# Kernel optimization log

Measured on AMD Instinct MI355X. Metric: run time of the kernel, lower is better.

## Reference

```python
import jax, jax.numpy as jnp
import numpy as np

B, S, DIM, HEADS = 4, 2048, 1024, 16
SCALE = float((DIM // HEADS) ** 0.5)  # sqrt(d_k) = 8.0
EPS = 1e-5


def _ln(h, g, b):
    m = jnp.mean(h, axis=-1, keepdims=True)
    v = jnp.mean((h - m) ** 2, axis=-1, keepdims=True)
    return (h - m) * jax.lax.rsqrt(v + EPS) * g + b


def setup_inputs() -> dict:
    key = jax.random.key(0)
    ks = jax.random.split(key, 16)
    w = lambda k: jax.random.normal(k, (DIM, DIM), jnp.float32) * 0.02
    vec = lambda k: jax.random.normal(k, (DIM,), jnp.float32) * 0.02
    return {
        "x": jax.random.normal(ks[0], (B, S, DIM), jnp.float32),
        "Wq": w(ks[1]), "bq": vec(ks[2]),
        "Wk": w(ks[3]), "bk": vec(ks[4]),
        "Wv": w(ks[5]), "bv": vec(ks[6]),
        "g_at": 1.0 + vec(ks[7]), "b_at": vec(ks[8]),
        "g_ln": 1.0 + vec(ks[9]), "b_ln": vec(ks[10]),
        "W1": w(ks[11]), "c1": vec(ks[12]),
        "W2": w(ks[13]), "c2": vec(ks[14]),
    }


def reference(x, Wq, bq, Wk, bk, Wv, bv, g_at, b_at, g_ln, b_ln, W1, c1, W2, c2):
    # --- MultiHeadAttention (single-head math: no head reshape in source) ---
    Q = x @ Wq + bq                                   # [B,S,D]
    K = x @ Wk + bk
    V = x @ Wv + bv
    scores = jax.nn.softmax(jnp.einsum('bqd,bkd->bqk', Q, K) / SCALE, axis=-1)
    at = _ln(jnp.einsum('bqk,bkd->bqd', scores, V) + x, g_at, b_at)
    # --- EncoderStack ---
    h = _ln(at + x, g_ln, b_ln)
    res = h
    # note: source's `if i != len(self.ffn)` is always True -> GELU on every layer
    h = jax.nn.gelu(h @ W1 + c1, approximate=False)
    h = jax.nn.gelu(h @ W2 + c2, approximate=False)
    return _ln(h + res, g_ln, b_ln)
```

## Files before the change

### kernel.cpp

```cpp
#include <hip/hip_runtime.h>
#include <cstdint>
#include <cstddef>

#define DIMN 1024
#define SEQ  2048
#define NBAT 4
#define TOKS (NBAT * SEQ)

typedef unsigned short u16;
typedef unsigned int   u32;

typedef __bf16 bf16x8 __attribute__((ext_vector_type(8)));
typedef float  f32x4  __attribute__((ext_vector_type(4)));

#define AS1 __attribute__((address_space(1)))
#define AS3 __attribute__((address_space(3)))


__device__ __forceinline__ u16 f2b(float f) {
  union { float f; u32 u; } v; v.f = f;
  u32 r = v.u + 0x7fffu + ((v.u >> 16) & 1u);
  return (u16)(r >> 16);
}

__device__ __forceinline__ float gelu_exact(float v) {
  return 0.5f * v * (1.0f + erff(v * 0.70710678118654752f));
}

__device__ __forceinline__ void blk_sum2(float& a, float& b, float* sm) {
  #pragma unroll
  for (int o = 32; o >= 1; o >>= 1) {
    a += __shfl_xor(a, o, 64);
    b += __shfl_xor(b, o, 64);
  }
  int w = threadIdx.x >> 6;
  if ((threadIdx.x & 63) == 0) { sm[w] = a; sm[4 + w] = b; }
  __syncthreads();
  a = sm[0] + sm[1] + sm[2] + sm[3];
  b = sm[4] + sm[5] + sm[6] + sm[7];
  __syncthreads();
}

__device__ __forceinline__ float blk_max(float a, float* sm) {
  #pragma unroll
  for (int o = 32; o >= 1; o >>= 1) a = fmaxf(a, __shfl_xor(a, o, 64));
  int w = threadIdx.x >> 6;
  if ((threadIdx.x & 63) == 0) sm[w] = a;
  __syncthreads();
  float r = fmaxf(fmaxf(sm[0], sm[1]), fmaxf(sm[2], sm[3]));
  __syncthreads();
  return r;
}

__device__ __forceinline__ float blk_sum1(float a, float* sm) {
  #pragma unroll
  for (int o = 32; o >= 1; o >>= 1) a += __shfl_xor(a, o, 64);
  int w = threadIdx.x >> 6;
  if ((threadIdx.x & 63) == 0) sm[w] = a;
  __syncthreads();
  float r = sm[0] + sm[1] + sm[2] + sm[3];
  __syncthreads();
  return r;
}


__global__ __launch_bounds__(256) void conv_x(const float* __restrict__ x,
                                              u16* __restrict__ xb) {
  size_t i = ((size_t)blockIdx.x * 256 + threadIdx.x) * 4;
  float4 v = *(const float4*)(x + i);
  uint2 o;
  o.x = (u32)f2b(v.x) | ((u32)f2b(v.y) << 16);
  o.y = (u32)f2b(v.z) | ((u32)f2b(v.w) << 16);
  *(uint2*)(xb + i) = o;
}

__global__ __launch_bounds__(256) void transpose_w5(
    const float* __restrict__ Wq, const float* __restrict__ Wk,
    const float* __restrict__ Wv, const float* __restrict__ W1,
    const float* __restrict__ W2,
    u16* __restrict__ WqT, u16* __restrict__ WkT, u16* __restrict__ WvT,
    u16* __restrict__ W1T, u16* __restrict__ W2T)
{
  const float* W; u16* T;
  switch (blockIdx.z) {
    case 0: W = Wq; T = WqT; break;
    case 1: W = Wk; T = WkT; break;
    case 2: W = Wv; T = WvT; break;
    case 3: W = W1; T = W1T; break;
    default: W = W2; T = W2T; break;
  }
  __shared__ float t[32][33];
  int tx = threadIdx.x, ty = threadIdx.y;
  int k0 = blockIdx.x * 32, n0 = blockIdx.y * 32;
  #pragma unroll
  for (int j = 0; j < 32; j += 8)
    t[ty + j][tx] = W[(size_t)(k0 + ty + j) * DIMN + n0 + tx];
  __syncthreads();
  #pragma unroll
  for (int j = 0; j < 32; j += 8)
    T[(size_t)(n0 + ty + j) * DIMN + k0 + tx] = f2b(t[tx][ty + j]);
}

template <int EPI>
__global__ __launch_bounds__(256) void gemm_bt(
    const u16* __restrict__ A, const u16* __restrict__ Bm,
    float* __restrict__ Cf, u16* __restrict__ Cb,
    const float* __restrict__ bias,
    int M, int N, int K, int ldc,
    size_t sA, size_t sB, size_t sC)
{
  __shared__ u16 As[128 * 64];
  __shared__ u16 Bs[128 * 64];

  const int tid  = threadIdx.x;
  const int bm0  = blockIdx.x * 128;
  const int bn0  = blockIdx.y * 128;
  A  += (size_t)blockIdx.z * sA;
  Bm += (size_t)blockIdx.z * sB;
  const int wave = tid >> 6, lane = tid & 63;
  const int wm   = (wave >> 1) * 64, wn = (wave & 1) * 64;
  const int l16  = lane & 15, quad = lane >> 4;

  f32x4 acc[4][4] = {};

  for (int k0 = 0; k0 < K; k0 += 64) {
    #pragma unroll
    for (int j = 0; j < 4; ++j) {
      const int c  = wave * 256 + j * 64 + lane;
      const int r  = c >> 3;
      const int cg = (c & 7) ^ (r & 7);
      const u16* gA = A  + (size_t)(bm0 + r) * K + k0 + cg * 8;
      const u16* gB = Bm + (size_t)(bn0 + r) * K + k0 + cg * 8;
      u16* lA = As + (wave * 4 + j) * 512;
      u16* lB = Bs + (wave * 4 + j) * 512;
      __builtin_amdgcn_global_load_lds((const AS1 void*)gA, (AS3 void*)lA, 16, 0, 0);
      __builtin_amdgcn_global_load_lds((const AS1 void*)gB, (AS3 void*)lB, 16, 0, 0);
    }
    __syncthreads();

    #pragma unroll
    for (int kk = 0; kk < 64; kk += 32) {
      const int kc = kk >> 3;
      const int sw = l16 & 7;
      bf16x8 af[4], bfr[4];
      #pragma unroll
      for (int t = 0; t < 4; ++t) {
        const int row = wm + t * 16 + l16;
        af[t] = *(const bf16x8*)(&As[row * 64 + (((kc + quad) ^ sw) << 3)]);
      }
      #pragma unroll
      for (int t = 0; t < 4; ++t) {
        const int row = wn + t * 16 + l16;
        bfr[t] = *(const bf16x8*)(&Bs[row * 64 + (((kc + quad) ^ sw) << 3)]);
      }
      #pragma unroll
      for (int mt = 0; mt < 4; ++mt)
        #pragma unroll
        for (int nt = 0; nt < 4; ++nt)
          acc[mt][nt] = __builtin_amdgcn_mfma_f32_16x16x32_bf16(
              af[mt], bfr[nt], acc[mt][nt], 0, 0, 0);
    }
    __syncthreads();
  }

  float* Cfz = Cf + (size_t)blockIdx.z * sC;
  u16*   Cbz = Cb + (size_t)blockIdx.z * sC;

  #pragma unroll
  for (int mt = 0; mt < 4; ++mt) {
    int grow0 = bm0 + wm + mt * 16 + quad * 4;
    #pragma unroll
    for (int nt = 0; nt < 4; ++nt) {
      int gcol = bn0 + wn + nt * 16 + l16;
      float bv = (EPI != 0) ? bias[gcol] : 0.0f;
      #pragma unroll
      for (int r = 0; r < 4; ++r) {
        float v  = acc[mt][nt][r] + bv;
        int grow = grow0 + r;
        if (EPI == 0) {
          Cfz[(size_t)grow * ldc + gcol] = v;
        } else if (EPI == 1) {
          Cbz[(size_t)grow * ldc + gcol] = f2b(v);
        } else if (EPI == 2) {
          Cbz[(size_t)((grow >> 11) * DIMN + gcol) * SEQ + (grow & 2047)] = f2b(v);
        } else if (EPI == 4) {
          Cbz[(size_t)grow * ldc + gcol] = f2b(gelu_exact(v));
        } else {
          Cfz[(size_t)grow * ldc + gcol] = gelu_exact(v);
        }
      }
    }
  }
}

__global__ __launch_bounds__(256) void softmax_rows(const float* __restrict__ Sc,
                                                    u16* __restrict__ P) {
  __shared__ float sm[8];
  int row = blockIdx.x, t = threadIdx.x;
  const float* s = Sc + (size_t)row * SEQ;
  float v[8];
  float mx = -1e30f;
  #pragma unroll
  for (int i = 0; i < 8; ++i) {
    v[i] = s[t + i * 256] * 0.125f;
    mx = fmaxf(mx, v[i]);
  }
  mx = blk_max(mx, sm);
  float sum = 0.0f;
  #pragma unroll
  for (int i = 0; i < 8; ++i) { v[i] = __expf(v[i] - mx); sum += v[i]; }
  sum = blk_sum1(sum, sm);
  float inv = 1.0f / sum;
  u16* p = P + (size_t)row * SEQ;
  #pragma unroll
  for (int i = 0; i < 8; ++i) p[t + i * 256] = f2b(v[i] * inv);
}

__global__ __launch_bounds__(256) void ln1_fused(
    const float* __restrict__ attn, const float* __restrict__ x,
    const float* __restrict__ g_at, const float* __restrict__ b_at,
    const float* __restrict__ g_ln, const float* __restrict__ b_ln,
    float* __restrict__ hres, u16* __restrict__ hb)
{
  __shared__ float sm[8];
  int row = blockIdx.x, t = threadIdx.x;
  size_t base = (size_t)row * DIMN;
  float y[4], xr[4];
  float s = 0.0f, s2 = 0.0f;
  #pragma unroll
  for (int i = 0; i < 4; ++i) {
    int c = t + i * 256;
    xr[i] = x[base + c];
    y[i]  = attn[base + c] + xr[i];
    s += y[i]; s2 += y[i] * y[i];
  }
  blk_sum2(s, s2, sm);
  float m  = s * (1.0f / DIMN);
  float rs = rsqrtf(s2 * (1.0f / DIMN) - m * m + 1e-5f);
  float z[4];
  s = 0.0f; s2 = 0.0f;
  #pragma unroll
  for (int i = 0; i < 4; ++i) {
    int c = t + i * 256;
    float at = (y[i] - m) * rs * g_at[c] + b_at[c];
    z[i] = at + xr[i];
    s += z[i]; s2 += z[i] * z[i];
  }
  blk_sum2(s, s2, sm);
  float m2  = s * (1.0f / DIMN);
  float rs2 = rsqrtf(s2 * (1.0f / DIMN) - m2 * m2 + 1e-5f);
  #pragma unroll
  for (int i = 0; i < 4; ++i) {
    int c = t + i * 256;
    float h = (z[i] - m2) * rs2 * g_ln[c] + b_ln[c];
    hres[base + c] = h;
    hb[base + c]   = f2b(h);
  }
}

__global__ __launch_bounds__(256) void ln2_final(
    const float* __restrict__ u, const float* __restrict__ hres,
    const float* __restrict__ g, const float* __restrict__ bb,
    float* __restrict__ out)
{
  __shared__ float sm[8];
  int row = blockIdx.x, t = threadIdx.x;
  size_t base = (size_t)row * DIMN;
  float y[4];
  float s = 0.0f, s2 = 0.0f;
  #pragma unroll
  for (int i = 0; i < 4; ++i) {
    int c = t + i * 256;
    y[i] = u[base + c] + hres[base + c];
    s += y[i]; s2 += y[i] * y[i];
  }
  blk_sum2(s, s2, sm);
  float m  = s * (1.0f / DIMN);
  float rs = rsqrtf(s2 * (1.0f / DIMN) - m * m + 1e-5f);
  #pragma unroll
  for (int i = 0; i < 4; ++i) {
    int c = t + i * 256;
    out[base + c] = (y[i] - m) * rs * g[c] + bb[c];
  }
}


extern "C" void kernel_launch(void* const* d_in, const int* in_sizes, int n_in,
                              void* d_out, int out_size, void* d_ws, size_t ws_size,
                              hipStream_t stream)
{
  const float* x    = (const float*)d_in[0];
  const float* Wq   = (const float*)d_in[1];
  const float* bq   = (const float*)d_in[2];
  const float* Wk   = (const float*)d_in[3];
  const float* bk   = (const float*)d_in[4];
  const float* Wv   = (const float*)d_in[5];
  const float* bv   = (const float*)d_in[6];
  const float* g_at = (const float*)d_in[7];
  const float* b_at = (const float*)d_in[8];
  const float* g_ln = (const float*)d_in[9];
  const float* b_ln = (const float*)d_in[10];
  const float* W1   = (const float*)d_in[11];
  const float* c1   = (const float*)d_in[12];
  const float* W2   = (const float*)d_in[13];
  const float* c2   = (const float*)d_in[14];
  float* out = (float*)d_out;

  char* ws = (char*)d_ws;
  const size_t MB = 1u << 20;
  const bool big = ws_size >= 172 * MB;

  u16* xb  = (u16*)(ws + 0 * MB);
  u16* W1T = (u16*)(ws + 16 * MB);
  u16* W2T = (u16*)(ws + 18 * MB);
  u16* WqT = (u16*)(ws + 20 * MB);
  u16* WkT = (u16*)(ws + 22 * MB);
  u16* WvT = (u16*)(ws + 24 * MB);
  u16* Qb  = (u16*)(ws + 26 * MB);
  u16* Kb  = (u16*)(ws + 42 * MB);
  u16* VT  = (u16*)(ws + 58 * MB);
  u16* hb  = Qb;
  u16* tb  = Kb;

  conv_x<<<(TOKS * DIMN) / 1024, 256, 0, stream>>>(x, xb);
  transpose_w5<<<dim3(32, 32, 5), dim3(32, 8), 0, stream>>>(
      Wq, Wk, Wv, W1, W2, WqT, WkT, WvT, W1T, W2T);

  gemm_bt<1><<<dim3(64, 8), 256, 0, stream>>>(xb, WqT, nullptr, Qb, bq,
                                              TOKS, DIMN, DIMN, DIMN, 0, 0, 0);
  gemm_bt<1><<<dim3(64, 8), 256, 0, stream>>>(xb, WkT, nullptr, Kb, bk,
                                              TOKS, DIMN, DIMN, DIMN, 0, 0, 0);
  gemm_bt<2><<<dim3(64, 8), 256, 0, stream>>>(xb, WvT, nullptr, VT, bv,
                                              TOKS, DIMN, DIMN, DIMN, 0, 0, 0);

  float* attn;
  float* hres;

  if (big) {
    float* Sc = (float*)(ws + 74 * MB);
    u16*   Pb = (u16*) (ws + 138 * MB);
    attn = (float*)(ws + 74 * MB);
    hres = (float*)(ws + 106 * MB);

    gemm_bt<0><<<dim3(16, 16, NBAT), 256, 0, stream>>>(
        Qb, Kb, Sc, nullptr, nullptr, SEQ, SEQ, DIMN, SEQ,
        (size_t)SEQ * DIMN, (size_t)SEQ * DIMN, (size_t)SEQ * SEQ);
    softmax_rows<<<TOKS, 256, 0, stream>>>(Sc, Pb);
    gemm_bt<0><<<dim3(16, 8, NBAT), 256, 0, stream>>>(
        Pb, VT, attn, nullptr, nullptr, SEQ, DIMN, SEQ, DIMN,
        (size_t)SEQ * SEQ, (size_t)DIMN * SEQ, (size_t)SEQ * DIMN);
  } else {
    float* Sc = (float*)(ws + 0 * MB);
    u16*   Pb = (u16*) (ws + 74 * MB);
    attn = (float*)(ws + 82 * MB);
    hres = (float*)(ws + 114 * MB);
    for (int b = 0; b < NBAT; ++b) {
      const size_t tok_off = (size_t)b * SEQ * DIMN;
      gemm_bt<0><<<dim3(16, 16), 256, 0, stream>>>(
          Qb + tok_off, Kb + tok_off, Sc, nullptr, nullptr,
          SEQ, SEQ, DIMN, SEQ, 0, 0, 0);
      softmax_rows<<<SEQ, 256, 0, stream>>>(Sc, Pb);
      gemm_bt<0><<<dim3(16, 8), 256, 0, stream>>>(
          Pb, VT + (size_t)b * DIMN * SEQ, attn + tok_off, nullptr, nullptr,
          SEQ, DIMN, SEQ, DIMN, 0, 0, 0);
    }
  }

  ln1_fused<<<TOKS, 256, 0, stream>>>(attn, x, g_at, b_at, g_ln, b_ln, hres, hb);

  gemm_bt<4><<<dim3(64, 8), 256, 0, stream>>>(hb, W1T, nullptr, tb, c1,
                                              TOKS, DIMN, DIMN, DIMN, 0, 0, 0);
  gemm_bt<5><<<dim3(64, 8), 256, 0, stream>>>(tb, W2T, attn, nullptr, c2,
                                              TOKS, DIMN, DIMN, DIMN, 0, 0, 0);

  ln2_final<<<TOKS, 256, 0, stream>>>(attn, hres, g_ln, b_ln, out);
}
```

Baseline: 422.5 us.

## Fuse QKV GEMM, store intermediates in bf16, swizzle block order, vectorize LN

Merges the three Q/K/V projections into one GEMM over a concatenated weight, and moves the V transpose into a separate kernel. Scores, attention output, residual and FFN outputs are stored as bf16 instead of fp32, which roughly halves intermediate memory traffic for softmax and the layernorms. The LN and softmax kernels also switch to vectorized loads and stores. GEMM blocks are remapped with an XCD-style index swizzle. The trade-off is lower precision: bf16 scores before softmax, x read back from bf16 for the residual, and the hres residual kept in bf16.

```diff
diff --git a/kernel.cpp b/kernel.cpp
--- a/kernel.cpp
+++ b/kernel.cpp
@@ -21,6 +21,11 @@
   union { float f; u32 u; } v; v.f = f;
   u32 r = v.u + 0x7fffu + ((v.u >> 16) & 1u);
   return (u16)(r >> 16);
+}
+
+__device__ __forceinline__ float b2f(u16 b) {
+  union { u32 u; float f; } v; v.u = ((u32)b) << 16;
+  return v.f;
 }
 
 __device__ __forceinline__ float gelu_exact(float v) {
@@ -78,16 +83,15 @@
     const float* __restrict__ Wq, const float* __restrict__ Wk,
     const float* __restrict__ Wv, const float* __restrict__ W1,
     const float* __restrict__ W2,
-    u16* __restrict__ WqT, u16* __restrict__ WkT, u16* __restrict__ WvT,
-    u16* __restrict__ W1T, u16* __restrict__ W2T)
+    u16* __restrict__ Wqkv, u16* __restrict__ W1T, u16* __restrict__ W2T)
 {
   const float* W; u16* T;
   switch (blockIdx.z) {
-    case 0: W = Wq; T = WqT; break;
-    case 1: W = Wk; T = WkT; break;
-    case 2: W = Wv; T = WvT; break;
-    case 3: W = W1; T = W1T; break;
-    default: W = W2; T = W2T; break;
+    case 0: W = Wq; T = Wqkv;                      break;
+    case 1: W = Wk; T = Wqkv + 1 * DIMN * DIMN;    break;
+    case 2: W = Wv; T = Wqkv + 2 * DIMN * DIMN;    break;
+    case 3: W = W1; T = W1T;                       break;
+    default: W = W2; T = W2T;                      break;
   }
   __shared__ float t[32][33];
   int tx = threadIdx.x, ty = threadIdx.y;
@@ -101,20 +105,43 @@
     T[(size_t)(n0 + ty + j) * DIMN + k0 + tx] = f2b(t[tx][ty + j]);
 }
 
+__global__ __launch_bounds__(256) void transpose_v(const u16* __restrict__ Vb,
+                                                   u16* __restrict__ VT) {
+  __shared__ u16 t[32][33];
+  int tx = threadIdx.x, ty = threadIdx.y;
+  int d0 = blockIdx.x * 32, t0 = blockIdx.y * 32;
+  const u16* src = Vb + (size_t)blockIdx.z * SEQ * DIMN;
+  u16*       dst = VT + (size_t)blockIdx.z * DIMN * SEQ;
+  #pragma unroll
+  for (int j = 0; j < 32; j += 8)
+    t[ty + j][tx] = src[(size_t)(t0 + ty + j) * DIMN + d0 + tx];
+  __syncthreads();
+  #pragma unroll
+  for (int j = 0; j < 32; j += 8)
+    dst[(size_t)(d0 + ty + j) * SEQ + t0 + tx] = t[tx][ty + j];
+}
+
 template <int EPI>
 __global__ __launch_bounds__(256) void gemm_bt(
     const u16* __restrict__ A, const u16* __restrict__ Bm,
-    float* __restrict__ Cf, u16* __restrict__ Cb,
-    const float* __restrict__ bias,
+    u16* __restrict__ Cb, u16* __restrict__ Cb2, u16* __restrict__ Cb3,
+    const float* __restrict__ bias, const float* __restrict__ bias2,
+    const float* __restrict__ bias3,
     int M, int N, int K, int ldc,
     size_t sA, size_t sB, size_t sC)
 {
   __shared__ u16 As[128 * 64];
   __shared__ u16 Bs[128 * 64];
 
-  const int tid  = threadIdx.x;
-  const int bm0  = blockIdx.x * 128;
-  const int bn0  = blockIdx.y * 128;
+  const int tid = threadIdx.x;
+
+  const int Tt   = gridDim.x * gridDim.y;
+  const int id   = blockIdx.y * gridDim.x + blockIdx.x;
+  const int per  = Tt >> 3;
+  const int flat = (id & 7) * per + (id >> 3);
+  const int bm0  = (flat % gridDim.x) * 128;
+  const int bn0  = (flat / gridDim.x) * 128;
+
   A  += (size_t)blockIdx.z * sA;
   Bm += (size_t)blockIdx.z * sB;
   const int wave = tid >> 6, lane = tid & 63;
@@ -163,8 +190,7 @@
     __syncthreads();
   }
 
-  float* Cfz = Cf + (size_t)blockIdx.z * sC;
-  u16*   Cbz = Cb + (size_t)blockIdx.z * sC;
+  u16* Cbz = Cb + (size_t)blockIdx.z * sC;
 
   #pragma unroll
   for (int mt = 0; mt < 4; ++mt) {
@@ -172,66 +198,79 @@
     #pragma unroll
     for (int nt = 0; nt < 4; ++nt) {
       int gcol = bn0 + wn + nt * 16 + l16;
-      float bv = (EPI != 0) ? bias[gcol] : 0.0f;
-      #pragma unroll
-      for (int r = 0; r < 4; ++r) {
-        float v  = acc[mt][nt][r] + bv;
-        int grow = grow0 + r;
-        if (EPI == 0) {
-          Cfz[(size_t)grow * ldc + gcol] = v;
-        } else if (EPI == 1) {
-          Cbz[(size_t)grow * ldc + gcol] = f2b(v);
-        } else if (EPI == 2) {
-          Cbz[(size_t)((grow >> 11) * DIMN + gcol) * SEQ + (grow & 2047)] = f2b(v);
-        } else if (EPI == 4) {
-          Cbz[(size_t)grow * ldc + gcol] = f2b(gelu_exact(v));
-        } else {
-          Cfz[(size_t)grow * ldc + gcol] = gelu_exact(v);
-        }
+      if (EPI == 3) {
+        const int seg = gcol >> 10;
+        const int col = gcol & 1023;
+        const float* bp = (seg == 0) ? bias : (seg == 1) ? bias2 : bias3;
+        u16*         cp = (seg == 0) ? Cb   : (seg == 1) ? Cb2   : Cb3;
+        float bv = bp[col];
+        #pragma unroll
+        for (int r = 0; r < 4; ++r)
+          cp[(size_t)(grow0 + r) * ldc + col] = f2b(acc[mt][nt][r] + bv);
+      } else if (EPI == 4) {
+        float bv = bias[gcol];
+        #pragma unroll
+        for (int r = 0; r < 4; ++r)
+          Cbz[(size_t)(grow0 + r) * ldc + gcol] =
+              f2b(gelu_exact(acc[mt][nt][r] + bv));
+      } else {
+        #pragma unroll
+        for (int r = 0; r < 4; ++r)
+          Cbz[(size_t)(grow0 + r) * ldc + gcol] = f2b(acc[mt][nt][r]);
       }
     }
   }
 }
 
-__global__ __launch_bounds__(256) void softmax_rows(const float* __restrict__ Sc,
+__global__ __launch_bounds__(256) void softmax_rows(const u16* __restrict__ Sc,
                                                     u16* __restrict__ P) {
   __shared__ float sm[8];
   int row = blockIdx.x, t = threadIdx.x;
-  const float* s = Sc + (size_t)row * SEQ;
+  const u16* s = Sc + (size_t)row * SEQ;
+  uint4 raw = *(const uint4*)(s + t * 8);
   float v[8];
+  #pragma unroll
+  for (int m = 0; m < 4; ++m) {
+    u32 w = ((const u32*)&raw)[m];
+    v[2 * m]     = b2f((u16)(w & 0xffff)) * 0.125f;
+    v[2 * m + 1] = b2f((u16)(w >> 16)) * 0.125f;
+  }
   float mx = -1e30f;
   #pragma unroll
-  for (int i = 0; i < 8; ++i) {
-    v[i] = s[t + i * 256] * 0.125f;
-    mx = fmaxf(mx, v[i]);
-  }
+  for (int i = 0; i < 8; ++i) mx = fmaxf(mx, v[i]);
   mx = blk_max(mx, sm);
   float sum = 0.0f;
   #pragma unroll
   for (int i = 0; i < 8; ++i) { v[i] = __expf(v[i] - mx); sum += v[i]; }
   sum = blk_sum1(sum, sm);
   float inv = 1.0f / sum;
-  u16* p = P + (size_t)row * SEQ;
-  #pragma unroll
-  for (int i = 0; i < 8; ++i) p[t + i * 256] = f2b(v[i] * inv);
+  uint4 o;
+  #pragma unroll
+  for (int m = 0; m < 4; ++m)
+    ((u32*)&o)[m] = (u32)f2b(v[2 * m] * inv) | ((u32)f2b(v[2 * m + 1] * inv) << 16);
+  *(uint4*)(P + (size_t)row * SEQ + t * 8) = o;
 }
 
 __global__ __launch_bounds__(256) void ln1_fused(
-    const float* __restrict__ attn, const float* __restrict__ x,
+    const u16* __restrict__ attn, const u16* __restrict__ xb,
     const float* __restrict__ g_at, const float* __restrict__ b_at,
     const float* __restrict__ g_ln, const float* __restrict__ b_ln,
-    float* __restrict__ hres, u16* __restrict__ hb)
+    u16* __restrict__ hres)
 {
   __shared__ float sm[8];
   int row = blockIdx.x, t = threadIdx.x;
   size_t base = (size_t)row * DIMN;
+  uint2 ar = *(const uint2*)(attn + base + t * 4);
+  uint2 xr4 = *(const uint2*)(xb + base + t * 4);
   float y[4], xr[4];
   float s = 0.0f, s2 = 0.0f;
   #pragma unroll
   for (int i = 0; i < 4; ++i) {
-    int c = t + i * 256;
-    xr[i] = x[base + c];
-    y[i]  = attn[base + c] + xr[i];
+    u32 aw = ((const u32*)&ar)[i >> 1];
+    u32 xw = ((const u32*)&xr4)[i >> 1];
+    float av = b2f((u16)((i & 1) ? (aw >> 16) : (aw & 0xffff)));
+    xr[i]    = b2f((u16)((i & 1) ? (xw >> 16) : (xw & 0xffff)));
+    y[i] = av + xr[i];
     s += y[i]; s2 += y[i] * y[i];
   }
   blk_sum2(s, s2, sm);
@@ -241,7 +280,7 @@
   s = 0.0f; s2 = 0.0f;
   #pragma unroll
   for (int i = 0; i < 4; ++i) {
-    int c = t + i * 256;
+    int c = t * 4 + i;
     float at = (y[i] - m) * rs * g_at[c] + b_at[c];
     z[i] = at + xr[i];
     s += z[i]; s2 += z[i] * z[i];
@@ -249,39 +288,47 @@
   blk_sum2(s, s2, sm);
   float m2  = s * (1.0f / DIMN);
   float rs2 = rsqrtf(s2 * (1.0f / DIMN) - m2 * m2 + 1e-5f);
-  #pragma unroll
-  for (int i = 0; i < 4; ++i) {
-    int c = t + i * 256;
-    float h = (z[i] - m2) * rs2 * g_ln[c] + b_ln[c];
-    hres[base + c] = h;
-    hb[base + c]   = f2b(h);
-  }
+  uint2 o;
+  #pragma unroll
+  for (int i = 0; i < 2; ++i) {
+    int c = t * 4 + 2 * i;
+    float h0 = (z[2 * i]     - m2) * rs2 * g_ln[c]     + b_ln[c];
+    float h1 = (z[2 * i + 1] - m2) * rs2 * g_ln[c + 1] + b_ln[c + 1];
+    ((u32*)&o)[i] = (u32)f2b(h0) | ((u32)f2b(h1) << 16);
+  }
+  *(uint2*)(hres + base + t * 4) = o;
 }
 
 __global__ __launch_bounds__(256) void ln2_final(
-    const float* __restrict__ u, const float* __restrict__ hres,
+    const u16* __restrict__ u, const u16* __restrict__ hres,
     const float* __restrict__ g, const float* __restrict__ bb,
     float* __restrict__ out)
 {
   __shared__ float sm[8];
   int row = blockIdx.x, t = threadIdx.x;
   size_t base = (size_t)row * DIMN;
+  uint2 ur = *(const uint2*)(u + base + t * 4);
+  uint2 hr = *(const uint2*)(hres + base + t * 4);
   float y[4];
   float s = 0.0f, s2 = 0.0f;
   #pragma unroll
   for (int i = 0; i < 4; ++i) {
-    int c = t + i * 256;
-    y[i] = u[base + c] + hres[base + c];
+    u32 uw = ((const u32*)&ur)[i >> 1];
+    u32 hw = ((const u32*)&hr)[i >> 1];
+    float uv = b2f((u16)((i & 1) ? (uw >> 16) : (uw & 0xffff)));
+    float hv = b2f((u16)((i & 1) ? (hw >> 16) : (hw & 0xffff)));
+    y[i] = uv + hv;
     s += y[i]; s2 += y[i] * y[i];
   }
   blk_sum2(s, s2, sm);
   float m  = s * (1.0f / DIMN);
   float rs = rsqrtf(s2 * (1.0f / DIMN) - m * m + 1e-5f);
-  #pragma unroll
-  for (int i = 0; i < 4; ++i) {
-    int c = t + i * 256;
-    out[base + c] = (y[i] - m) * rs * g[c] + bb[c];
-  }
+  float4 o;
+  o.x = (y[0] - m) * rs * g[t * 4 + 0] + bb[t * 4 + 0];
+  o.y = (y[1] - m) * rs * g[t * 4 + 1] + bb[t * 4 + 1];
+  o.z = (y[2] - m) * rs * g[t * 4 + 2] + bb[t * 4 + 2];
+  o.w = (y[3] - m) * rs * g[t * 4 + 3] + bb[t * 4 + 3];
+  *(float4*)(out + base + t * 4) = o;
 }
 
 
@@ -308,70 +355,49 @@
 
   char* ws = (char*)d_ws;
   const size_t MB = 1u << 20;
-  const bool big = ws_size >= 172 * MB;
-
-  u16* xb  = (u16*)(ws + 0 * MB);
-  u16* W1T = (u16*)(ws + 16 * MB);
-  u16* W2T = (u16*)(ws + 18 * MB);
-  u16* WqT = (u16*)(ws + 20 * MB);
-  u16* WkT = (u16*)(ws + 22 * MB);
-  u16* WvT = (u16*)(ws + 24 * MB);
-  u16* Qb  = (u16*)(ws + 26 * MB);
-  u16* Kb  = (u16*)(ws + 42 * MB);
-  u16* VT  = (u16*)(ws + 58 * MB);
-  u16* hb  = Qb;
-  u16* tb  = Kb;
+  u16* xb    = (u16*)(ws + 0 * MB);
+  u16* W1T   = (u16*)(ws + 16 * MB);
+  u16* W2T   = (u16*)(ws + 18 * MB);
+  u16* WqkvT = (u16*)(ws + 20 * MB);
+  u16* Qb    = (u16*)(ws + 26 * MB);
+  u16* Kb    = (u16*)(ws + 42 * MB);
+  u16* Vb    = (u16*)(ws + 58 * MB);
+  u16* VT    = (u16*)(ws + 74 * MB);
+  u16* Sc    = (u16*)(ws + 90 * MB);
+  u16* attn  = (u16*)(ws + 90 * MB);
+  u16* hres  = (u16*)(ws + 106 * MB);
+  u16* Pb    = (u16*)(ws + 122 * MB);
+  u16* tb    = Kb;
+  u16* ub    = Vb;
 
   conv_x<<<(TOKS * DIMN) / 1024, 256, 0, stream>>>(x, xb);
   transpose_w5<<<dim3(32, 32, 5), dim3(32, 8), 0, stream>>>(
-      Wq, Wk, Wv, W1, W2, WqT, WkT, WvT, W1T, W2T);
-
-  gemm_bt<1><<<dim3(64, 8), 256, 0, stream>>>(xb, WqT, nullptr, Qb, bq,
-                                              TOKS, DIMN, DIMN, DIMN, 0, 0, 0);
-  gemm_bt<1><<<dim3(64, 8), 256, 0, stream>>>(xb, WkT, nullptr, Kb, bk,
-                                              TOKS, DIMN, DIMN, DIMN, 0, 0, 0);
-  gemm_bt<2><<<dim3(64, 8), 256, 0, stream>>>(xb, WvT, nullptr, VT, bv,
-                                              TOKS, DIMN, DIMN, DIMN, 0, 0, 0);
-
-  float* attn;
-  float* hres;
-
-  if (big) {
-    float* Sc = (float*)(ws + 74 * MB);
-    u16*   Pb = (u16*) (ws + 138 * MB);
-    attn = (float*)(ws + 74 * MB);
-    hres = (float*)(ws + 106 * MB);
-
-    gemm_bt<0><<<dim3(16, 16, NBAT), 256, 0, stream>>>(
-        Qb, Kb, Sc, nullptr, nullptr, SEQ, SEQ, DIMN, SEQ,
-        (size_t)SEQ * DIMN, (size_t)SEQ * DIMN, (size_t)SEQ * SEQ);
-    softmax_rows<<<TOKS, 256, 0, stream>>>(Sc, Pb);
-    gemm_bt<0><<<dim3(16, 8, NBAT), 256, 0, stream>>>(
-        Pb, VT, attn, nullptr, nullptr, SEQ, DIMN, SEQ, DIMN,
-        (size_t)SEQ * SEQ, (size_t)DIMN * SEQ, (size_t)SEQ * DIMN);
-  } else {
-    float* Sc = (float*)(ws + 0 * MB);
-    u16*   Pb = (u16*) (ws + 74 * MB);
-    attn = (float*)(ws + 82 * MB);
-    hres = (float*)(ws + 114 * MB);
-    for (int b = 0; b < NBAT; ++b) {
-      const size_t tok_off = (size_t)b * SEQ * DIMN;
-      gemm_bt<0><<<dim3(16, 16), 256, 0, stream>>>(
-          Qb + tok_off, Kb + tok_off, Sc, nullptr, nullptr,
-          SEQ, SEQ, DIMN, SEQ, 0, 0, 0);
-      softmax_rows<<<SEQ, 256, 0, stream>>>(Sc, Pb);
-      gemm_bt<0><<<dim3(16, 8), 256, 0, stream>>>(
-          Pb, VT + (size_t)b * DIMN * SEQ, attn + tok_off, nullptr, nullptr,
-          SEQ, DIMN, SEQ, DIMN, 0, 0, 0);
-    }
-  }
-
-  ln1_fused<<<TOKS, 256, 0, stream>>>(attn, x, g_at, b_at, g_ln, b_ln, hres, hb);
-
-  gemm_bt<4><<<dim3(64, 8), 256, 0, stream>>>(hb, W1T, nullptr, tb, c1,
-                                              TOKS, DIMN, DIMN, DIMN, 0, 0, 0);
-  gemm_bt<5><<<dim3(64, 8), 256, 0, stream>>>(tb, W2T, attn, nullptr, c2,
-                                              TOKS, DIMN, DIMN, DIMN, 0, 0, 0);
-
-  ln2_final<<<TOKS, 256, 0, stream>>>(attn, hres, g_ln, b_ln, out);
-}
+      Wq, Wk, Wv, W1, W2, WqkvT, W1T, W2T);
+
+  gemm_bt<3><<<dim3(64, 24), 256, 0, stream>>>(
+      xb, WqkvT, Qb, Kb, Vb, bq, bk, bv,
+      TOKS, 3 * DIMN, DIMN, DIMN, 0, 0, 0);
+
+  transpose_v<<<dim3(32, 64, NBAT), dim3(32, 8), 0, stream>>>(Vb, VT);
+
+  gemm_bt<6><<<dim3(16, 16, NBAT), 256, 0, stream>>>(
+      Qb, Kb, Sc, nullptr, nullptr, nullptr, nullptr, nullptr,
+      SEQ, SEQ, DIMN, SEQ,
+      (size_t)SEQ * DIMN, (size_t)SEQ * DIMN, (size_t)SEQ * SEQ);
+  softmax_rows<<<TOKS, 256, 0, stream>>>(Sc, Pb);
+  gemm_bt<6><<<dim3(16, 8, NBAT), 256, 0, stream>>>(
+      Pb, VT, attn, nullptr, nullptr, nullptr, nullptr, nullptr,
+      SEQ, DIMN, SEQ, DIMN,
+      (size_t)SEQ * SEQ, (size_t)DIMN * SEQ, (size_t)SEQ * DIMN);
+
+  ln1_fused<<<TOKS, 256, 0, stream>>>(attn, xb, g_at, b_at, g_ln, b_ln, hres);
+
+  gemm_bt<4><<<dim3(64, 8), 256, 0, stream>>>(
+      hres, W1T, tb, nullptr, nullptr, c1, nullptr, nullptr,
+      TOKS, DIMN, DIMN, DIMN, 0, 0, 0);
+  gemm_bt<4><<<dim3(64, 8), 256, 0, stream>>>(
+      tb, W2T, ub, nullptr, nullptr, c2, nullptr, nullptr,
+      TOKS, DIMN, DIMN, DIMN, 0, 0, 0);
+
+  ln2_final<<<TOKS, 256, 0, stream>>>(ub, hres, g_ln, b_ln, out);
+}
```

After: 407.6 us. -3.5%, faster.
